# Kernel tuning notes

Measured on AMD Instinct MI355X. Metric: run time of the kernel, lower is better.

The kernel has to match this reference:

```python
import jax, jax.numpy as jnp
import numpy as np


def setup_inputs() -> dict:
    key = jax.random.key(0)
    k1, k2 = jax.random.split(key)
    B, H, S = 16, 512, 1024          # batch, hidden=nd*embed_dim, seqlen
    ND, ED, K = 4, 128, 4096         # nd, embed_dim, num_embed
    inputs = jax.random.normal(k1, (B, H, S), dtype=jnp.float32)
    embeddings = jax.random.normal(k2, (ND, ED, K), dtype=jnp.float32)
    return {"inputs": inputs, "embeddings": embeddings}


def reference(inputs, embeddings):
    # VectorQuant.forward with soft_train=False, gsoftmax=False, EMA=False (VQ-VAE straight-through path)
    commit_cost = 0.25
    B, H, S = inputs.shape
    ND, ED, K = embeddings.shape
    # stack_enc_outputs: (B, H, S) -> (B*S, nd, embed_dim) via contiguous view (C-order reshape)
    enc = inputs.reshape(B * S, ND, ED)
    x2 = jnp.sum(enc * enc, axis=2, keepdims=True)            # (BS, nd, 1)
    e2 = jnp.sum(embeddings * embeddings, axis=1)[None]       # (1, nd, K)
    cross = jnp.einsum('dhk,bdh->bdk', embeddings, enc)       # (BS, nd, K)
    distances = x2 + e2 - 2.0 * cross
    # per-token, per-chunk nearest code
    latents = jnp.argmin(distances, axis=2).T                 # (nd, BS)
    # gather codebook vectors: embeddings[d][:, latents[d]] -> (nd, ED, BS)
    encodings = jnp.take_along_axis(embeddings, latents[:, None, :], axis=2)
    # split_outputs: (nd, ED, B*S) -> (B, H, S) via contiguous view (C-order reshape)
    encodings = encodings.reshape(B, H, S)
    # straight-through estimator
    output = inputs + jax.lax.stop_gradient(encodings) - jax.lax.stop_gradient(inputs)
    commit_loss = jnp.mean((inputs - jax.lax.stop_gradient(encodings)) ** 2)
    loss = commit_cost * commit_loss
    kl = jnp.asarray(0, dtype=jnp.int32)
    return (output, loss, commit_loss, kl)
```

## Files before the change

kernel.cpp:

```cpp
#include <hip/hip_runtime.h>

#define ND 4
#define ED 128
#define KCODES 4096
#define NTOK 16384
#define HID 512
#define NTOT (ND*ED*NTOK)

#define MARGIN 2.0e-3f
#define FLAG_CAP 16384

typedef __attribute__((ext_vector_type(8))) short short8v;
typedef __attribute__((ext_vector_type(4))) float float4v;

#define GLDS16(g, l) __builtin_amdgcn_global_load_lds( \
    (const __attribute__((address_space(1))) unsigned int*)(g), \
    (__attribute__((address_space(3))) unsigned int*)(l), 16, 0, 0)

__device__ __forceinline__ unsigned short bf16h(float x) {
    unsigned u = __float_as_uint(x);
    return (unsigned short)((u + 0x7fffu + ((u >> 16) & 1u)) >> 16);
}
__device__ __forceinline__ float bf16f(unsigned short h) {
    return __uint_as_float(((unsigned)h) << 16);
}

__global__ __launch_bounds__(256) void e2split_kernel(const float* __restrict__ emb,
        float* __restrict__ e2g, unsigned short* __restrict__ bfrag,
        int* __restrict__ flag_cnt) {
    __shared__ float Tf[128][17];
    const int tile = blockIdx.x;
    const int d    = blockIdx.y;
    const int tid  = threadIdx.x;
    const int k0   = tile * 16;
    if (tile == 0 && d == 0 && tid == 0) *flag_cnt = 0;
    {
        int e = tid >> 1, half = tid & 1;
        const float* src = emb + ((size_t)d * ED + e) * KCODES + k0 + half * 8;
        float4 v0 = *(const float4*)(src);
        float4 v1 = *(const float4*)(src + 4);
        float* dst = &Tf[e][half * 8];
        dst[0] = v0.x; dst[1] = v0.y; dst[2] = v0.z; dst[3] = v0.w;
        dst[4] = v1.x; dst[5] = v1.y; dst[6] = v1.z; dst[7] = v1.w;
    }
    __syncthreads();
    if (tid < 16) {
        float s = 0.f;
        for (int e = 0; e < ED; ++e) {
            float v = Tf[e][tid];
            s = __fadd_rn(s, __fmul_rn(v, v));
        }
        e2g[d * KCODES + k0 + tid] = s;
    }
    #pragma unroll
    for (int q = 0; q < 2; ++q) {
        int c    = q * 256 + tid;
        int arr  = c >> 8;
        int rem  = c & 255;
        int code = rem >> 4;
        int kpos = rem & 15;
        int e0   = (kpos ^ code) * 8;
        short8v v;
        #pragma unroll
        for (int j = 0; j < 8; ++j) {
            float x = Tf[e0 + j][code];
            unsigned short hb = bf16h(x);
            v[j] = arr ? (short)bf16h(x - bf16f(hb)) : (short)hb;
        }
        size_t idx = ((size_t)(d * 256 + tile)) * 4096 + arr * 2048 + code * 128 + kpos * 8;
        *(short8v*)(bfrag + idx) = v;
    }
}

__global__ __launch_bounds__(256, 2)
void argmin_mfma_kernel(const float* __restrict__ in,
        const unsigned short* __restrict__ bfrag, const float* __restrict__ e2g,
        unsigned long long* __restrict__ pk, unsigned* __restrict__ pm2) {
    __shared__ __align__(16) char LB[40960];

    const int l   = blockIdx.x;
    const int r8  = l & 7;
    const int d   = r8 >> 1;
    const int h   = r8 & 1;
    const int tI  = l >> 3;
    const int t0  = tI * 128;

    const int tid  = threadIdx.x;
    const int w    = tid >> 6;
    const int lane = tid & 63;
    const int l15  = lane & 15;
    const int lk8  = lane >> 4;

    float* e2p = (float*)(LB + 32768);
    #pragma unroll
    for (int i = 0; i < 8; ++i) {
        int idx = i * 256 + tid;
        e2p[idx] = e2g[d * KCODES + h * 2048 + idx] + 512.0f;
    }

    short8v ahf[2][4], alf[2][4];
    #pragma unroll
    for (int rt = 0; rt < 2; ++rt) {
        const float* ap = in + (size_t)(t0 + w * 32 + rt * 16 + l15) * HID + d * ED + lk8 * 8;
        #pragma unroll
        for (int ks = 0; ks < 4; ++ks) {
            float4 v0 = *(const float4*)(ap + ks * 32);
            float4 v1 = *(const float4*)(ap + ks * 32 + 4);
            float vv[8] = {v0.x, v0.y, v0.z, v0.w, v1.x, v1.y, v1.z, v1.w};
            short8v hv, lv;
            #pragma unroll
            for (int j = 0; j < 8; ++j) {
                unsigned short hb = bf16h(vv[j]);
                hv[j] = (short)hb;
                lv[j] = (short)bf16h(vv[j] - bf16f(hb));
            }
            ahf[rt][ks] = hv; alf[rt][ks] = lv;
        }
    }

    int fo[4];
    #pragma unroll
    for (int ks = 0; ks < 4; ++ks)
        fo[ks] = l15 * 256 + (((ks * 4 + lk8) ^ l15) * 16);

    const char* sb = (const char*)bfrag + ((size_t)(d * 256 + h * 128)) * 8192 + tid * 16;

    #pragma unroll
    for (int t = 0; t < 2; ++t) {
        GLDS16(sb + t * 8192,        LB + t * 8192 + w * 1024);
        GLDS16(sb + t * 8192 + 4096, LB + t * 8192 + 4096 + w * 1024);
    }
    __syncthreads();

    unsigned m1[2][4], m2[2][4];
    int bk[2][4];
    #pragma unroll
    for (int rt = 0; rt < 2; ++rt)
        #pragma unroll
        for (int r = 0; r < 4; ++r) { m1[rt][r] = 0xFFFFFFFFu; m2[rt][r] = 0xFFFFFFFFu; bk[rt][r] = 0; }

    #pragma unroll 4
    for (int s = 0; s < 128; ++s) {
        if (s < 126) {
            const char* sp = sb + (size_t)(s + 2) * 8192;
            char* dp = LB + ((s + 2) & 3) * 8192 + w * 1024;
            GLDS16(sp,        dp);
            GLDS16(sp + 4096, dp + 4096);
        }
        const char* cur = LB + (s & 3) * 8192;
        const float e2v = e2p[s * 16 + l15];

        float4v aP[2] = {{0,0,0,0},{0,0,0,0}};
        float4v aQ[2] = {{0,0,0,0},{0,0,0,0}};
        __builtin_amdgcn_s_setprio(1);
        #pragma unroll
        for (int ks = 0; ks < 4; ++ks) {
            short8v bh = *(const short8v*)(cur + fo[ks]);
            short8v bl = *(const short8v*)(cur + 4096 + fo[ks]);
            aP[0] = __builtin_amdgcn_mfma_f32_16x16x32_bf16(ahf[0][ks], bh, aP[0], 0, 0, 0);
            aP[1] = __builtin_amdgcn_mfma_f32_16x16x32_bf16(ahf[1][ks], bh, aP[1], 0, 0, 0);
            aP[0] = __builtin_amdgcn_mfma_f32_16x16x32_bf16(alf[0][ks], bh, aP[0], 0, 0, 0);
            aP[1] = __builtin_amdgcn_mfma_f32_16x16x32_bf16(alf[1][ks], bh, aP[1], 0, 0, 0);
            aQ[0] = __builtin_amdgcn_mfma_f32_16x16x32_bf16(ahf[0][ks], bl, aQ[0], 0, 0, 0);
            aQ[1] = __builtin_amdgcn_mfma_f32_16x16x32_bf16(ahf[1][ks], bl, aQ[1], 0, 0, 0);
        }
        __builtin_amdgcn_s_setprio(0);
        #pragma unroll
        for (int rt = 0; rt < 2; ++rt) {
            #pragma unroll
            for (int r = 0; r < 4; ++r) {
                float cs = aP[rt][r] + aQ[rt][r];
                float dv = __fmaf_rn(-2.0f, cs, e2v);
                unsigned kk = __float_as_uint(dv);
                unsigned mo = m1[rt][r];
                unsigned mx = mo > kk ? mo : kk;
                m2[rt][r] = m2[rt][r] < mx ? m2[rt][r] : mx;
                if (kk < mo) { bk[rt][r] = s; m1[rt][r] = kk; }
            }
        }
        if (s < 126)        asm volatile("s_waitcnt vmcnt(2)" ::: "memory");
        else if (s == 126)  asm volatile("s_waitcnt vmcnt(0)" ::: "memory");
        __builtin_amdgcn_s_barrier();
    }

    #pragma unroll
    for (int rt = 0; rt < 2; ++rt) {
        #pragma unroll
        for (int r = 0; r < 4; ++r) {
            unsigned long long key = ((unsigned long long)m1[rt][r] << 32) |
                                     (unsigned)(h * 2048 + bk[rt][r] * 16 + l15);
            unsigned mm2 = m2[rt][r];
            #pragma unroll
            for (int m = 1; m <= 8; m <<= 1) {
                unsigned long long ok = __shfl_xor(key, m, 64);
                unsigned om = __shfl_xor(mm2, m, 64);
                unsigned loser = (ok < key) ? (unsigned)(key >> 32) : (unsigned)(ok >> 32);
                key = ok < key ? ok : key;
                unsigned t2 = om < loser ? om : loser;
                mm2 = mm2 < t2 ? mm2 : t2;
            }
            if (l15 == 0) {
                int tok = d * NTOK + t0 + w * 32 + rt * 16 + lk8 * 4 + r;
                pk[(size_t)h * 65536 + tok] = key;
                pm2[(size_t)h * 65536 + tok] = mm2;
            }
        }
    }
}

__global__ __launch_bounds__(256) void merge_kernel(
        const unsigned long long* __restrict__ pk, const unsigned* __restrict__ pm2,
        int* __restrict__ lat, int* __restrict__ flag_cnt, int* __restrict__ flag_list) {
    int tok = blockIdx.x * 256 + threadIdx.x;
    unsigned long long ka = pk[tok], kb = pk[65536 + tok];
    unsigned m2a = pm2[tok], m2b = pm2[65536 + tok];
    bool aw = ka < kb;
    unsigned long long kw = aw ? ka : kb;
    unsigned loser1 = (unsigned)((aw ? kb : ka) >> 32);
    unsigned m2w = aw ? m2a : m2b;
    unsigned B2 = m2w < loser1 ? m2w : loser1;
    lat[tok] = (int)(kw & 0xFFFFu);
    float gap = __uint_as_float(B2) - __uint_as_float((unsigned)(kw >> 32));
    if (gap < MARGIN) {
        int slot = atomicAdd(flag_cnt, 1);
        if (slot < FLAG_CAP) flag_list[slot] = tok;
    }
}

__global__ __launch_bounds__(256) void repair_kernel(const float* __restrict__ in,
        const float* __restrict__ emb, const float* __restrict__ e2g,
        const int* __restrict__ flag_cnt, const int* __restrict__ flag_list,
        int* __restrict__ lat) {
    __shared__ float xs[ED];
    __shared__ float rd[256];
    __shared__ int   rk[256];
    int n = *flag_cnt;
    if (n > FLAG_CAP) n = FLAG_CAP;
    for (int idx = blockIdx.x; idx < n; idx += gridDim.x) {
        int tok = flag_list[idx];
        int d = tok >> 14;
        int t = tok & (NTOK - 1);
        __syncthreads();
        if (threadIdx.x < ED) xs[threadIdx.x] = in[(size_t)t * HID + d * ED + threadIdx.x];
        __syncthreads();
        float x2v = 0.f;
        for (int e = 0; e < ED; ++e) x2v = __fadd_rn(x2v, __fmul_rn(xs[e], xs[e]));
        const float* __restrict__ embd = emb + (size_t)d * ED * KCODES;
        float bd = 3.0e38f; int bkk = 0;
        for (int j = 0; j < 16; ++j) {
            int k = threadIdx.x + j * 256;
            float acc = 0.f;
            #pragma unroll 16
            for (int e = 0; e < ED; ++e)
                acc = __fmaf_rn(xs[e], embd[(size_t)e * KCODES + k], acc);
            float dist = __fsub_rn(__fadd_rn(x2v, e2g[d * KCODES + k]),
                                   __fmul_rn(2.0f, acc));
            if (dist < bd) { bd = dist; bkk = k; }
        }
        rd[threadIdx.x] = bd; rk[threadIdx.x] = bkk;
        __syncthreads();
        for (int w = 128; w > 0; w >>= 1) {
            if (threadIdx.x < w) {
                float od = rd[threadIdx.x + w]; int ok = rk[threadIdx.x + w];
                if (od < rd[threadIdx.x] || (od == rd[threadIdx.x] && ok < rk[threadIdx.x])) {
                    rd[threadIdx.x] = od; rk[threadIdx.x] = ok;
                }
            }
            __syncthreads();
        }
        if (threadIdx.x == 0) lat[tok] = rk[0];
    }
}

__global__ __launch_bounds__(256) void gather_kernel(const float* __restrict__ in,
        const float* __restrict__ emb, const int* __restrict__ lat,
        float* __restrict__ out, float* __restrict__ partial) {
    int tid  = threadIdx.x;
    int base = blockIdx.x * 1024 + tid * 4;
    int d = base >> 21;
    int e = (base >> 14) & 127;
    int t = base & (NTOK - 1);
    const int4 kk = *(const int4*)(lat + d * NTOK + t);
    const float* __restrict__ row = emb + ((size_t)(d * ED + e)) * KCODES;
    float enc[4];
    enc[0] = row[kk.x]; enc[1] = row[kk.y]; enc[2] = row[kk.z]; enc[3] = row[kk.w];
    const float4 x = *(const float4*)(in + base);
    const float xv[4] = {x.x, x.y, x.z, x.w};
    float4 ov; float* o = (float*)&ov;
    float s = 0.f;
    #pragma unroll
    for (int i = 0; i < 4; ++i) {
        o[i] = __fsub_rn(__fadd_rn(xv[i], enc[i]), xv[i]);
        float df = xv[i] - enc[i];
        s = __fmaf_rn(df, df, s);
    }
    *(float4*)(out + base) = ov;
    #pragma unroll
    for (int off = 32; off > 0; off >>= 1) s += __shfl_down(s, off, 64);
    __shared__ float wsum[4];
    if ((tid & 63) == 0) wsum[tid >> 6] = s;
    __syncthreads();
    if (tid == 0) partial[blockIdx.x] = wsum[0] + wsum[1] + wsum[2] + wsum[3];
}

__global__ __launch_bounds__(256) void finalize_kernel(const float* __restrict__ partial,
                                                       float* __restrict__ out_tail) {
    __shared__ double sh[256];
    double s = 0.0;
    for (int i = threadIdx.x; i < 8192; i += 256) s += (double)partial[i];
    sh[threadIdx.x] = s;
    __syncthreads();
    for (int w = 128; w > 0; w >>= 1) {
        if (threadIdx.x < w) sh[threadIdx.x] += sh[threadIdx.x + w];
        __syncthreads();
    }
    if (threadIdx.x == 0) {
        double mean = sh[0] / (double)NTOT;
        out_tail[0] = (float)(0.25 * mean);
        out_tail[1] = (float)mean;
        ((int*)out_tail)[2] = 0;
    }
}

extern "C" void kernel_launch(void* const* d_in, const int* in_sizes, int n_in,
                              void* d_out, int out_size, void* d_ws, size_t ws_size,
                              hipStream_t stream) {
    const float* in  = (const float*)d_in[0];
    const float* emb = (const float*)d_in[1];
    float* out = (float*)d_out;
    char* ws = (char*)d_ws;

    int*   lat       = (int*)ws;
    float* e2g       = (float*)(ws + 262144);
    float* partial   = (float*)(ws + 327680);
    int*   flag_cnt  = (int*)(ws + 360448);
    int*   flag_list = (int*)(ws + 360452);
    unsigned long long* pk  = (unsigned long long*)(ws + 458752);
    unsigned*           pm2 = (unsigned*)(ws + 1572864);
    unsigned short* bfrag = (unsigned short*)(ws + 2097152);

    hipLaunchKernelGGL(e2split_kernel, dim3(256, 4), dim3(256), 0, stream,
                       emb, e2g, bfrag, flag_cnt);
    hipLaunchKernelGGL(argmin_mfma_kernel, dim3(1024), dim3(256), 0, stream,
                       in, bfrag, e2g, pk, pm2);
    hipLaunchKernelGGL(merge_kernel, dim3(256), dim3(256), 0, stream,
                       pk, pm2, lat, flag_cnt, flag_list);
    hipLaunchKernelGGL(repair_kernel, dim3(64), dim3(256), 0, stream,
                       in, emb, e2g, flag_cnt, flag_list, lat);
    hipLaunchKernelGGL(gather_kernel, dim3(NTOT / 1024), dim3(256), 0, stream,
                       in, emb, lat, out, partial);
    hipLaunchKernelGGL(finalize_kernel, dim3(1), dim3(256), 0, stream, partial, out + NTOT);
}
```

Measured before the change: 279.5 us.

## Deepen codebook LDS prefetch to three stages and register-prefetch B fragments

Measured after the change: 273.8 us. 2.0% less time.

```diff
diff --git a/kernel.cpp b/kernel.cpp
--- a/kernel.cpp
+++ b/kernel.cpp
@@ -126,11 +126,19 @@
     const char* sb = (const char*)bfrag + ((size_t)(d * 256 + h * 128)) * 8192 + tid * 16;
 
     #pragma unroll
-    for (int t = 0; t < 2; ++t) {
+    for (int t = 0; t < 3; ++t) {
         GLDS16(sb + t * 8192,        LB + t * 8192 + w * 1024);
         GLDS16(sb + t * 8192 + 4096, LB + t * 8192 + 4096 + w * 1024);
     }
+    asm volatile("s_waitcnt vmcnt(2)" ::: "memory");
     __syncthreads();
+
+    short8v rbh[4], rbl[4];
+    #pragma unroll
+    for (int ks = 0; ks < 4; ++ks) {
+        rbh[ks] = *(const short8v*)(LB + fo[ks]);
+        rbl[ks] = *(const short8v*)(LB + 4096 + fo[ks]);
+    }
 
     unsigned m1[2][4], m2[2][4];
     int bk[2][4];
@@ -140,31 +148,35 @@
         for (int r = 0; r < 4; ++r) { m1[rt][r] = 0xFFFFFFFFu; m2[rt][r] = 0xFFFFFFFFu; bk[rt][r] = 0; }
 
     #pragma unroll 4
-    for (int s = 0; s < 128; ++s) {
-        if (s < 126) {
-            const char* sp = sb + (size_t)(s + 2) * 8192;
-            char* dp = LB + ((s + 2) & 3) * 8192 + w * 1024;
+    for (int j = 0; j < 128; ++j) {
+        if (j < 125) {
+            const char* sp = sb + (size_t)(j + 3) * 8192;
+            char* dp = LB + ((j + 3) & 3) * 8192 + w * 1024;
             GLDS16(sp,        dp);
             GLDS16(sp + 4096, dp + 4096);
         }
-        const char* cur = LB + (s & 3) * 8192;
-        const float e2v = e2p[s * 16 + l15];
+        const float e2v = e2p[j * 16 + l15];
+        const char* nb = LB + ((j + 1) & 3) * 8192;
 
         float4v aP[2] = {{0,0,0,0},{0,0,0,0}};
         float4v aQ[2] = {{0,0,0,0},{0,0,0,0}};
-        __builtin_amdgcn_s_setprio(1);
-        #pragma unroll
-        for (int ks = 0; ks < 4; ++ks) {
-            short8v bh = *(const short8v*)(cur + fo[ks]);
-            short8v bl = *(const short8v*)(cur + 4096 + fo[ks]);
-            aP[0] = __builtin_amdgcn_mfma_f32_16x16x32_bf16(ahf[0][ks], bh, aP[0], 0, 0, 0);
-            aP[1] = __builtin_amdgcn_mfma_f32_16x16x32_bf16(ahf[1][ks], bh, aP[1], 0, 0, 0);
-            aP[0] = __builtin_amdgcn_mfma_f32_16x16x32_bf16(alf[0][ks], bh, aP[0], 0, 0, 0);
-            aP[1] = __builtin_amdgcn_mfma_f32_16x16x32_bf16(alf[1][ks], bh, aP[1], 0, 0, 0);
-            aQ[0] = __builtin_amdgcn_mfma_f32_16x16x32_bf16(ahf[0][ks], bl, aQ[0], 0, 0, 0);
-            aQ[1] = __builtin_amdgcn_mfma_f32_16x16x32_bf16(ahf[1][ks], bl, aQ[1], 0, 0, 0);
-        }
-        __builtin_amdgcn_s_setprio(0);
+        #define KSTEP(ks) \
+            aP[0] = __builtin_amdgcn_mfma_f32_16x16x32_bf16(ahf[0][ks], rbh[ks], aP[0], 0, 0, 0); \
+            aP[1] = __builtin_amdgcn_mfma_f32_16x16x32_bf16(ahf[1][ks], rbh[ks], aP[1], 0, 0, 0); \
+            aP[0] = __builtin_amdgcn_mfma_f32_16x16x32_bf16(alf[0][ks], rbh[ks], aP[0], 0, 0, 0); \
+            aP[1] = __builtin_amdgcn_mfma_f32_16x16x32_bf16(alf[1][ks], rbh[ks], aP[1], 0, 0, 0); \
+            aQ[0] = __builtin_amdgcn_mfma_f32_16x16x32_bf16(ahf[0][ks], rbl[ks], aQ[0], 0, 0, 0); \
+            aQ[1] = __builtin_amdgcn_mfma_f32_16x16x32_bf16(ahf[1][ks], rbl[ks], aQ[1], 0, 0, 0); \
+            if (j < 127) { \
+                rbh[ks] = *(const short8v*)(nb + fo[ks]); \
+                rbl[ks] = *(const short8v*)(nb + 4096 + fo[ks]); \
+            }
+        KSTEP(0)
+        KSTEP(1)
+        KSTEP(2)
+        KSTEP(3)
+        #undef KSTEP
+
         #pragma unroll
         for (int rt = 0; rt < 2; ++rt) {
             #pragma unroll
@@ -175,11 +187,11 @@
                 unsigned mo = m1[rt][r];
                 unsigned mx = mo > kk ? mo : kk;
                 m2[rt][r] = m2[rt][r] < mx ? m2[rt][r] : mx;
-                if (kk < mo) { bk[rt][r] = s; m1[rt][r] = kk; }
-            }
-        }
-        if (s < 126)        asm volatile("s_waitcnt vmcnt(2)" ::: "memory");
-        else if (s == 126)  asm volatile("s_waitcnt vmcnt(0)" ::: "memory");
+                if (kk < mo) { bk[rt][r] = j; m1[rt][r] = kk; }
+            }
+        }
+        if (j < 124)  asm volatile("s_waitcnt vmcnt(2)" ::: "memory");
+        else          asm volatile("s_waitcnt vmcnt(0)" ::: "memory");
         __builtin_amdgcn_s_barrier();
     }
 
```

## Load codebook fragments directly to registers and double tokens per block

Applied to the files above, without the earlier changes.

Result: slower. 304.4 us (+8.9%).

```diff
diff --git a/kernel.cpp b/kernel.cpp
--- a/kernel.cpp
+++ b/kernel.cpp
@@ -12,10 +12,6 @@
 
 typedef __attribute__((ext_vector_type(8))) short short8v;
 typedef __attribute__((ext_vector_type(4))) float float4v;
-
-#define GLDS16(g, l) __builtin_amdgcn_global_load_lds( \
-    (const __attribute__((address_space(1))) unsigned int*)(g), \
-    (__attribute__((address_space(3))) unsigned int*)(l), 16, 0, 0)
 
 __device__ __forceinline__ unsigned short bf16h(float x) {
     unsigned u = __float_as_uint(x);
@@ -76,14 +72,14 @@
 void argmin_mfma_kernel(const float* __restrict__ in,
         const unsigned short* __restrict__ bfrag, const float* __restrict__ e2g,
         unsigned long long* __restrict__ pk, unsigned* __restrict__ pm2) {
-    __shared__ __align__(16) char LB[40960];
+    __shared__ float e2p[2048];
 
     const int l   = blockIdx.x;
     const int r8  = l & 7;
     const int d   = r8 >> 1;
     const int h   = r8 & 1;
     const int tI  = l >> 3;
-    const int t0  = tI * 128;
+    const int t0  = tI * 256;
 
     const int tid  = threadIdx.x;
     const int w    = tid >> 6;
@@ -91,17 +87,17 @@
     const int l15  = lane & 15;
     const int lk8  = lane >> 4;
 
-    float* e2p = (float*)(LB + 32768);
     #pragma unroll
     for (int i = 0; i < 8; ++i) {
         int idx = i * 256 + tid;
         e2p[idx] = e2g[d * KCODES + h * 2048 + idx] + 512.0f;
     }
-
-    short8v ahf[2][4], alf[2][4];
-    #pragma unroll
-    for (int rt = 0; rt < 2; ++rt) {
-        const float* ap = in + (size_t)(t0 + w * 32 + rt * 16 + l15) * HID + d * ED + lk8 * 8;
+    __syncthreads();
+
+    short8v ahf[4][4], alf[4][4];
+    #pragma unroll
+    for (int rt = 0; rt < 4; ++rt) {
+        const float* ap = in + (size_t)(t0 + w * 64 + rt * 16 + l15) * HID + d * ED + lk8 * 8;
         #pragma unroll
         for (int ks = 0; ks < 4; ++ks) {
             float4 v0 = *(const float4*)(ap + ks * 32);
@@ -123,68 +119,57 @@
     for (int ks = 0; ks < 4; ++ks)
         fo[ks] = l15 * 256 + (((ks * 4 + lk8) ^ l15) * 16);
 
-    const char* sb = (const char*)bfrag + ((size_t)(d * 256 + h * 128)) * 8192 + tid * 16;
-
-    #pragma unroll
-    for (int t = 0; t < 2; ++t) {
-        GLDS16(sb + t * 8192,        LB + t * 8192 + w * 1024);
-        GLDS16(sb + t * 8192 + 4096, LB + t * 8192 + 4096 + w * 1024);
-    }
-    __syncthreads();
-
-    unsigned m1[2][4], m2[2][4];
-    int bk[2][4];
-    #pragma unroll
-    for (int rt = 0; rt < 2; ++rt)
+    const char* sb = (const char*)bfrag + ((size_t)(d * 256 + h * 128)) * 8192;
+
+    unsigned m1[4][4], m2[4][4];
+    int bk[4][4];
+    #pragma unroll
+    for (int rt = 0; rt < 4; ++rt)
         #pragma unroll
         for (int r = 0; r < 4; ++r) { m1[rt][r] = 0xFFFFFFFFu; m2[rt][r] = 0xFFFFFFFFu; bk[rt][r] = 0; }
 
-    #pragma unroll 4
-    for (int s = 0; s < 128; ++s) {
-        if (s < 126) {
-            const char* sp = sb + (size_t)(s + 2) * 8192;
-            char* dp = LB + ((s + 2) & 3) * 8192 + w * 1024;
-            GLDS16(sp,        dp);
-            GLDS16(sp + 4096, dp + 4096);
-        }
-        const char* cur = LB + (s & 3) * 8192;
-        const float e2v = e2p[s * 16 + l15];
-
-        float4v aP[2] = {{0,0,0,0},{0,0,0,0}};
-        float4v aQ[2] = {{0,0,0,0},{0,0,0,0}};
-        __builtin_amdgcn_s_setprio(1);
+    short8v X[8];
+    #pragma unroll
+    for (int ks = 0; ks < 4; ++ks) {
+        X[ks]     = *(const short8v*)(sb + fo[ks]);
+        X[4 + ks] = *(const short8v*)(sb + 4096 + fo[ks]);
+    }
+
+    #pragma unroll 2
+    for (int j = 0; j < 128; ++j) {
+        const float e2v = e2p[j * 16 + l15];
+        const char* nb = sb + (size_t)(j + 1) * 8192;
+
+        float4v acc[4] = {{0,0,0,0},{0,0,0,0},{0,0,0,0},{0,0,0,0}};
         #pragma unroll
         for (int ks = 0; ks < 4; ++ks) {
-            short8v bh = *(const short8v*)(cur + fo[ks]);
-            short8v bl = *(const short8v*)(cur + 4096 + fo[ks]);
-            aP[0] = __builtin_amdgcn_mfma_f32_16x16x32_bf16(ahf[0][ks], bh, aP[0], 0, 0, 0);
-            aP[1] = __builtin_amdgcn_mfma_f32_16x16x32_bf16(ahf[1][ks], bh, aP[1], 0, 0, 0);
-            aP[0] = __builtin_amdgcn_mfma_f32_16x16x32_bf16(alf[0][ks], bh, aP[0], 0, 0, 0);
-            aP[1] = __builtin_amdgcn_mfma_f32_16x16x32_bf16(alf[1][ks], bh, aP[1], 0, 0, 0);
-            aQ[0] = __builtin_amdgcn_mfma_f32_16x16x32_bf16(ahf[0][ks], bl, aQ[0], 0, 0, 0);
-            aQ[1] = __builtin_amdgcn_mfma_f32_16x16x32_bf16(ahf[1][ks], bl, aQ[1], 0, 0, 0);
-        }
-        __builtin_amdgcn_s_setprio(0);
-        #pragma unroll
-        for (int rt = 0; rt < 2; ++rt) {
+            #pragma unroll
+            for (int rt = 0; rt < 4; ++rt) {
+                acc[rt] = __builtin_amdgcn_mfma_f32_16x16x32_bf16(ahf[rt][ks], X[ks], acc[rt], 0, 0, 0);
+                acc[rt] = __builtin_amdgcn_mfma_f32_16x16x32_bf16(alf[rt][ks], X[ks], acc[rt], 0, 0, 0);
+                acc[rt] = __builtin_amdgcn_mfma_f32_16x16x32_bf16(ahf[rt][ks], X[4 + ks], acc[rt], 0, 0, 0);
+            }
+            if (j < 127) {
+                X[ks]     = *(const short8v*)(nb + fo[ks]);
+                X[4 + ks] = *(const short8v*)(nb + 4096 + fo[ks]);
+            }
+        }
+        #pragma unroll
+        for (int rt = 0; rt < 4; ++rt) {
             #pragma unroll
             for (int r = 0; r < 4; ++r) {
-                float cs = aP[rt][r] + aQ[rt][r];
-                float dv = __fmaf_rn(-2.0f, cs, e2v);
+                float dv = __fmaf_rn(-2.0f, acc[rt][r], e2v);
                 unsigned kk = __float_as_uint(dv);
                 unsigned mo = m1[rt][r];
                 unsigned mx = mo > kk ? mo : kk;
                 m2[rt][r] = m2[rt][r] < mx ? m2[rt][r] : mx;
-                if (kk < mo) { bk[rt][r] = s; m1[rt][r] = kk; }
-            }
-        }
-        if (s < 126)        asm volatile("s_waitcnt vmcnt(2)" ::: "memory");
-        else if (s == 126)  asm volatile("s_waitcnt vmcnt(0)" ::: "memory");
-        __builtin_amdgcn_s_barrier();
-    }
-
-    #pragma unroll
-    for (int rt = 0; rt < 2; ++rt) {
+                if (kk < mo) { bk[rt][r] = j; m1[rt][r] = kk; }
+            }
+        }
+    }
+
+    #pragma unroll
+    for (int rt = 0; rt < 4; ++rt) {
         #pragma unroll
         for (int r = 0; r < 4; ++r) {
             unsigned long long key = ((unsigned long long)m1[rt][r] << 32) |
@@ -200,7 +185,7 @@
                 mm2 = mm2 < t2 ? mm2 : t2;
             }
             if (l15 == 0) {
-                int tok = d * NTOK + t0 + w * 32 + rt * 16 + lk8 * 4 + r;
+                int tok = d * NTOK + t0 + w * 64 + rt * 16 + lk8 * 4 + r;
                 pk[(size_t)h * 65536 + tok] = key;
                 pm2[(size_t)h * 65536 + tok] = mm2;
             }
@@ -341,7 +326,7 @@
 
     hipLaunchKernelGGL(e2split_kernel, dim3(256, 4), dim3(256), 0, stream,
                        emb, e2g, bfrag, flag_cnt);
-    hipLaunchKernelGGL(argmin_mfma_kernel, dim3(1024), dim3(256), 0, stream,
+    hipLaunchKernelGGL(argmin_mfma_kernel, dim3(512), dim3(256), 0, stream,
                        in, bfrag, e2g, pk, pm2);
     hipLaunchKernelGGL(merge_kernel, dim3(256), dim3(256), 0, stream,
                        pk, pm2, lat, flag_cnt, flag_list);
```
